# Performance work log

Measured on AMD Instinct MI355X. Metric: run time of the kernel, lower is better.

The kernel has to match this reference:

```python
import math
import jax, jax.numpy as jnp
import numpy as np

B, T, C, H = 4, 2048, 1024, 1024

def setup_inputs() -> dict:
    key = jax.random.key(0)
    kx, kk, kq, kv = jax.random.split(key, 4)
    s = 1.0 / math.sqrt(C)
    return {
        "x": jax.random.normal(kx, (B, T, C), dtype=jnp.float32),
        # torch Linear weight is [out, in]; store transposed [in, out] for x @ W
        "Wk": jax.random.uniform(kk, (C, H), dtype=jnp.float32, minval=-s, maxval=s),
        "Wq": jax.random.uniform(kq, (C, H), dtype=jnp.float32, minval=-s, maxval=s),
        "Wv": jax.random.uniform(kv, (C, H), dtype=jnp.float32, minval=-s, maxval=s),
    }

def reference(x, Wk, Wq, Wv):
    K = x @ Wk  # [B,T,H]
    Q = x @ Wq
    V = x @ Wv
    scale = 1.0 / math.sqrt(K.shape[-1])
    wei = jnp.einsum('bth,bsh->bts', Q, K) * scale  # [B,T,T]
    t = x.shape[1]
    causal = jnp.tril(jnp.ones((t, t), dtype=bool))
    wei = jnp.where(causal, wei, -jnp.inf)
    wei = jax.nn.softmax(wei, axis=-1)
    wei = jax.nn.relu(wei)  # no-op mathematically but kept for fidelity
    return jnp.einsum('bts,bsh->bth', wei, V)
```

## Files before the change

### kernel.cpp

```cpp
#include <hip/hip_runtime.h>

typedef _Float16 f16;
typedef _Float16 f16x8 __attribute__((ext_vector_type(8)));
typedef float    f32x4 __attribute__((ext_vector_type(4)));

#define AS3 __attribute__((address_space(3)))
#define AS1 __attribute__((address_space(1)))

static __device__ __forceinline__ void gld_lds16(const f16* g, f16* l) {
    __builtin_amdgcn_global_load_lds((const AS1 void*)g, (AS3 void*)l, 16, 0, 0);
}

static __device__ __forceinline__ unsigned pack_f16(float a, float b) {
    union { f16 h[2]; unsigned u; } p;
    p.h[0] = (f16)a; p.h[1] = (f16)b;
    return p.u;
}

__global__ void cvt_fused(const float* __restrict__ x, f16* __restrict__ xh,
                          const float* __restrict__ Wq, const float* __restrict__ Wk,
                          const float* __restrict__ Wv, f16* __restrict__ Wt) {
    __shared__ float tile[32][33];
    const int bid = blockIdx.x;
    if (bid < 4096) {
        int i = bid * 256 + threadIdx.x;
        const f32x4* xv = (const f32x4*)x;
        f32x4 a = xv[2 * i], b = xv[2 * i + 1];
        f16x8 h;
        h[0] = (f16)a[0]; h[1] = (f16)a[1]; h[2] = (f16)a[2]; h[3] = (f16)a[3];
        h[4] = (f16)b[0]; h[5] = (f16)b[1]; h[6] = (f16)b[2]; h[7] = (f16)b[3];
        ((f16x8*)xh)[i] = h;
    } else {
        int b2 = bid - 4096;
        int bx = b2 & 31, by = (b2 >> 5) & 31, bz = b2 >> 10;
        const float* W = bz == 0 ? Wq : (bz == 1 ? Wk : Wv);
        int tx = threadIdx.x & 31, ty = threadIdx.x >> 5;
        int n0 = bx * 32, k0 = by * 32;
#pragma unroll
        for (int r = 0; r < 4; ++r)
            tile[ty + r * 8][tx] = W[(size_t)(k0 + ty + r * 8) * 1024 + n0 + tx];
        __syncthreads();
        f16* o = Wt + (size_t)bz * 1024 * 1024;
#pragma unroll
        for (int r = 0; r < 4; ++r)
            o[(size_t)(n0 + ty + r * 8) * 1024 + k0 + tx] = (f16)tile[tx][ty + r * 8];
    }
}

#define KT 16

__global__ __launch_bounds__(512, 2)
void gemm256(const f16* __restrict__ Axh, const f16* __restrict__ Bw, f16* __restrict__ Cqk,
             const f16* __restrict__ Awv, const f16* __restrict__ Bxh, f16* __restrict__ CVt) {
    const int orig = blockIdx.x;
    const int wg = (orig & 7) * 48 + (orig >> 3);
    int m0, n0; const f16 *Ab, *Bb; f16* Cb;
    if (wg < 256) {
        m0 = (wg >> 3) * 256; n0 = (wg & 7) * 256;
        Ab = Axh; Bb = Bw; Cb = Cqk;
    } else {
        int t = wg - 256, bb = t >> 5, r = t & 31;
        m0 = (r >> 3) * 256; n0 = (r & 7) * 256;
        Ab = Awv; Bb = Bxh + (long)bb * 2048 * 1024; Cb = CVt + (long)bb * 1024 * 2048;
    }
    const int lda = 1024, ldb = 1024, ldc = 2048;

    __shared__ f16 lds[2 * 32768];

    const int tid = threadIdx.x;
    const int wave = tid >> 6, lane = tid & 63;
    const int q = lane >> 4, rr = lane & 15;
    const int wr = wave >> 2, wc = wave & 3;

    const int kcs = (((lane & 7) - (lane >> 3)) & 7) * 8;
    const f16* pA = Ab + (long)(m0 + (tid >> 3)) * lda + kcs;
    const f16* pB = Bb + (long)(n0 + (tid >> 3)) * ldb + kcs;
    const int ldsw = wave * 512;

    auto stageA = [&](int kt, int h, int buf) {
        f16* dst = lds + buf * 32768 + h * 8192 + ldsw;
        const f16* src = pA + (long)(h * 128) * lda + kt * 64;
        gld_lds16(src, dst);
        gld_lds16(src + (long)64 * lda, dst + 4096);
    };
    auto stageB = [&](int kt, int h, int buf) {
        f16* dst = lds + buf * 32768 + 16384 + h * 8192 + ldsw;
        const f16* src = pB + (long)(h * 128) * ldb + kt * 64;
        gld_lds16(src, dst);
        gld_lds16(src + (long)64 * ldb, dst + 4096);
    };

    f32x4 acc[8][4] = {};

    stageA(0, 0, 0); stageA(0, 1, 0); stageB(0, 0, 0); stageB(0, 1, 0);
    stageB(1 < KT ? 1 : KT - 1, 0, 1); stageB(1 < KT ? 1 : KT - 1, 1, 1);
    asm volatile("s_waitcnt vmcnt(4)" ::: "memory");
    __builtin_amdgcn_s_barrier();

    for (int u = 0; u < KT; ++u) {
        const int cur = u & 1;
        const f16* bA = lds + cur * 32768 + wr * 8192;
        const f16* bB = lds + cur * 32768 + 16384 + (wc >> 1) * 8192;
        const int brow = (wc & 1) * 64;
        const int ua = u + 1 < KT ? u + 1 : KT - 1;
        const int ub = u + 2 < KT ? u + 2 : KT - 1;
        const int bufA_ = (u + 1) & 1, bufB_ = cur;
        f16x8 bf[4][2];
#pragma unroll
        for (int p = 0; p < 4; ++p) {
            f16x8 a[2][2];
            if (p == 0) {
#pragma unroll
                for (int j = 0; j < 4; ++j)
#pragma unroll
                    for (int ks = 0; ks < 2; ++ks)
                        bf[j][ks] = *(const f16x8*)&bB[(brow + j * 16 + rr) * 64 + ((ks * 4 + q + rr) & 7) * 8];
            }
#pragma unroll
            for (int fi = 0; fi < 2; ++fi)
#pragma unroll
                for (int ks = 0; ks < 2; ++ks)
                    a[fi][ks] = *(const f16x8*)&bA[((p * 2 + fi) * 16 + rr) * 64 + ((ks * 4 + q + rr) & 7) * 8];
            if      (p == 0) stageA(ua, 0, bufA_);
            else if (p == 1) stageA(ua, 1, bufA_);
            else if (p == 2) stageB(ub, 0, bufB_);
            else             stageB(ub, 1, bufB_);
            __builtin_amdgcn_s_barrier();
            asm volatile("s_waitcnt lgkmcnt(0)" ::: "memory");
            __builtin_amdgcn_sched_barrier(0);
            __builtin_amdgcn_s_setprio(1);
#pragma unroll
            for (int ks = 0; ks < 2; ++ks)
#pragma unroll
                for (int fi = 0; fi < 2; ++fi)
#pragma unroll
                    for (int j = 0; j < 4; ++j)
                        acc[p * 2 + fi][j] = __builtin_amdgcn_mfma_f32_16x16x32_f16(
                            a[fi][ks], bf[j][ks], acc[p * 2 + fi][j], 0, 0, 0);
            __builtin_amdgcn_s_setprio(0);
            if (p == 3) asm volatile("s_waitcnt vmcnt(4)" ::: "memory");
            __builtin_amdgcn_s_barrier();
        }
    }
    asm volatile("s_waitcnt vmcnt(0)" ::: "memory");

#pragma unroll
    for (int i = 0; i < 8; ++i)
#pragma unroll
        for (int r2 = 0; r2 < 4; ++r2) {
            const long row = m0 + wr * 128 + i * 16 + q * 4 + r2;
#pragma unroll
            for (int j = 0; j < 4; ++j)
                Cb[row * ldc + n0 + wc * 64 + j * 16 + rr] = (f16)acc[i][j][r2];
        }
}

template <int MODE>
__global__ __launch_bounds__(256, 4)
void gemm128(const f16* __restrict__ A, int lda, long aStride,
             const f16* __restrict__ B, int ldb, long bStride,
             void* __restrict__ Cout, int ldc, long cStride,
             int ktiles, float scale,
             const f16* __restrict__ A2, const f16* __restrict__ B2,
             void* __restrict__ C2) {
    int bm, bn, bz = blockIdx.z;
    int m0, n0;
    const f16 *Ab, *Bb;
    char* Cb;

    if (MODE == 1) {
        int i = blockIdx.x;
        float ff = sqrtf(8.f * (float)i + 1.f);
        bm = (int)((ff - 1.f) * 0.5f);
        while ((bm + 1) * (bm + 2) / 2 <= i) ++bm;
        while (bm * (bm + 1) / 2 > i) --bm;
        bn = i - bm * (bm + 1) / 2;
        m0 = bm * 128; n0 = bn * 128;
        Ab = A + (long)bz * aStride;
        Bb = B + (long)bz * bStride;
        Cb = (char*)Cout + (long)bz * cStride * sizeof(f16);
    } else {
        bn = blockIdx.x; bm = gridDim.y - 1 - blockIdx.y;
        int lim = 4 * (bm + 1); if (lim < ktiles) ktiles = lim;
        m0 = bm * 128; n0 = bn * 128;
        Ab = A + (long)bz * aStride;
        Bb = B + (long)bz * bStride;
        Cb = (char*)Cout + (long)bz * cStride * sizeof(float);
    }

    __shared__ f16 lds[2 * 8192];

    const int tid = threadIdx.x;
    const int wave = tid >> 6, lane = tid & 63;
    const int q = lane >> 4, rr = lane & 15;
    const int wm = (wave >> 1) * 64, wn = (wave & 1) * 64;

    const int kcs = (((tid & 3) - (lane >> 4)) & 3) * 8;
    const f16* pA = Ab + (long)(m0 + (tid >> 2)) * lda + kcs;
    const f16* pB = Bb + (long)(n0 + (tid >> 2)) * ldb + kcs;

    auto stage = [&](int kt, int buf) {
        const int k0 = kt * 32;
        f16* lA = lds + buf * 8192 + wave * 512;
        f16* lB = lds + buf * 8192 + 4096 + wave * 512;
#pragma unroll
        for (int it = 0; it < 2; ++it) {
            gld_lds16(pA + (long)it * 64 * lda + k0, lA + it * 2048);
            gld_lds16(pB + (long)it * 64 * ldb + k0, lB + it * 2048);
        }
    };

    const int slotf = ((q + (rr >> 2)) & 3) * 8;

    f32x4 acc[4][4] = {};
    f32x4 accs[4] = {};
    f16x8 onef;
    const bool sumwave = (MODE == 2) && (wn == 0);
    if (MODE == 2) {
#pragma unroll
        for (int t = 0; t < 8; ++t) onef[t] = (f16)1.0f;
    }

    stage(0, 0);
    __syncthreads();

    for (int kt = 0; kt < ktiles; ++kt) {
        const int cur = kt & 1;
        if (kt + 1 < ktiles) stage(kt + 1, 1 - cur);
        const f16* bufA = lds + cur * 8192;
        const f16* bufB = bufA + 4096;
        f16x8 af[4], bf[4];
#pragma unroll
        for (int i = 0; i < 4; ++i)
            af[i] = *(const f16x8*)&bufA[(wm + i * 16 + rr) * 32 + slotf];
#pragma unroll
        for (int j = 0; j < 4; ++j)
            bf[j] = *(const f16x8*)&bufB[(wn + j * 16 + rr) * 32 + slotf];
#pragma unroll
        for (int i = 0; i < 4; ++i) {
#pragma unroll
            for (int j = 0; j < 4; ++j)
                acc[i][j] = __builtin_amdgcn_mfma_f32_16x16x32_f16(af[i], bf[j], acc[i][j], 0, 0, 0);
            if (sumwave)
                accs[i] = __builtin_amdgcn_mfma_f32_16x16x32_f16(af[i], onef, accs[i], 0, 0, 0);
        }
        __syncthreads();
    }

    float invr[4][4];
    if (MODE == 2) {
        float* rs = (float*)lds;
        if (sumwave && rr == 0) {
#pragma unroll
            for (int i = 0; i < 4; ++i)
#pragma unroll
                for (int r2 = 0; r2 < 4; ++r2)
                    rs[wm + i * 16 + q * 4 + r2] = accs[i][r2];
        }
        __syncthreads();
#pragma unroll
        for (int i = 0; i < 4; ++i)
#pragma unroll
            for (int r2 = 0; r2 < 4; ++r2)
                invr[i][r2] = 1.0f / rs[wm + i * 16 + q * 4 + r2];
    }

#pragma unroll
    for (int i = 0; i < 4; ++i) {
#pragma unroll
        for (int r2 = 0; r2 < 4; ++r2) {
            const int row = wm + i * 16 + q * 4 + r2;
#pragma unroll
            for (int j = 0; j < 4; ++j) {
                const int col = wn + j * 16 + rr;
                float v = acc[i][j][r2] * scale;
                long idx = (long)(m0 + row) * ldc + n0 + col;
                if (MODE == 1) {
                    v = __expf(v);
                    if (n0 + col > m0 + row) v = 0.f;
                    float vo = __shfl_xor(v, 1, 64);
                    if ((rr & 1) == 0)
                        *(unsigned*)((f16*)Cb + idx) = pack_f16(v, vo);
                } else {
                    v *= invr[i][r2];
                    float vo = __shfl_xor(v, 1, 64);
                    if ((rr & 1) == 0)
                        *(float2*)((float*)Cb + idx) = make_float2(v, vo);
                }
            }
        }
    }
}

extern "C" void kernel_launch(void* const* d_in, const int* in_sizes, int n_in,
                              void* d_out, int out_size, void* d_ws, size_t ws_size,
                              hipStream_t stream) {
    (void)in_sizes; (void)n_in; (void)out_size; (void)ws_size;
    const float* x  = (const float*)d_in[0];
    const float* Wk = (const float*)d_in[1];
    const float* Wq = (const float*)d_in[2];
    const float* Wv = (const float*)d_in[3];
    float* out = (float*)d_out;

    const long MB = 1l << 20;
    char* ws = (char*)d_ws;
    f16*   qk   = (f16*)(ws);
    f16*   Vt   = (f16*)(ws + 32 * MB);
    f16*   P    = (f16*)(ws + 48 * MB);
    f16*   xh   = (f16*)(ws + 81 * MB);
    f16*   Wt   = (f16*)(ws + 97 * MB);

    cvt_fused<<<7168, 256, 0, stream>>>(x, xh, Wq, Wk, Wv, Wt);

    gemm256<<<dim3(384), 512, 0, stream>>>(xh, Wt, qk,
                                           Wt + 2l * 1024 * 1024, xh, Vt);
    gemm128<1><<<dim3(136, 1, 4), 256, 0, stream>>>(qk, 2048, 2048l * 2048,
                                                    qk + 1024, 2048, 2048l * 2048,
                                                    P, 2048, 2048l * 2048, 32, 0.03125f,
                                                    nullptr, nullptr, nullptr);
    gemm128<2><<<dim3(8, 16, 4), 256, 0, stream>>>(P, 2048, 2048l * 2048,
                                                   Vt, 2048, 1024l * 2048,
                                                   out, 1024, 2048l * 1024, 64, 1.0f,
                                                   nullptr, nullptr, nullptr);
}
```

Baseline: 249.0 us.

## Move V projection into causal QK^T launch and remap block orders

The V^T = Wv^T·x^T projection tiles move out of the 256-wide projection GEMM and into the causal QK^T launch as extra 128x128 blocks. This balances the triangular QK^T grid with dense work and leaves gemm256 doing only the Q/K projection. Block indices in the QK^T and PV kernels are remapped with interleaving swizzles, meant to improve L2 locality and spread causal work across CUs. Epilogue stores drop the shuffle-and-pack path for plain scalar stores, which may reduce store efficiency.

```diff
diff --git a/kernel.cpp b/kernel.cpp
--- a/kernel.cpp
+++ b/kernel.cpp
@@ -9,12 +9,6 @@
 
 static __device__ __forceinline__ void gld_lds16(const f16* g, f16* l) {
     __builtin_amdgcn_global_load_lds((const AS1 void*)g, (AS3 void*)l, 16, 0, 0);
-}
-
-static __device__ __forceinline__ unsigned pack_f16(float a, float b) {
-    union { f16 h[2]; unsigned u; } p;
-    p.h[0] = (f16)a; p.h[1] = (f16)b;
-    return p.u;
 }
 
 __global__ void cvt_fused(const float* __restrict__ x, f16* __restrict__ xh,
@@ -50,19 +44,11 @@
 #define KT 16
 
 __global__ __launch_bounds__(512, 2)
-void gemm256(const f16* __restrict__ Axh, const f16* __restrict__ Bw, f16* __restrict__ Cqk,
-             const f16* __restrict__ Awv, const f16* __restrict__ Bxh, f16* __restrict__ CVt) {
+void gemm256(const f16* __restrict__ Axh, const f16* __restrict__ Bw, f16* __restrict__ Cqk) {
     const int orig = blockIdx.x;
-    const int wg = (orig & 7) * 48 + (orig >> 3);
-    int m0, n0; const f16 *Ab, *Bb; f16* Cb;
-    if (wg < 256) {
-        m0 = (wg >> 3) * 256; n0 = (wg & 7) * 256;
-        Ab = Axh; Bb = Bw; Cb = Cqk;
-    } else {
-        int t = wg - 256, bb = t >> 5, r = t & 31;
-        m0 = (r >> 3) * 256; n0 = (r & 7) * 256;
-        Ab = Awv; Bb = Bxh + (long)bb * 2048 * 1024; Cb = CVt + (long)bb * 1024 * 2048;
-    }
+    const int wg = (orig & 7) * 32 + (orig >> 3);
+    const int m0 = (wg >> 3) * 256, n0 = (wg & 7) * 256;
+    const f16* Ab = Axh; const f16* Bb = Bw; f16* Cb = Cqk;
     const int lda = 1024, ldb = 1024, ldc = 2048;
 
     __shared__ f16 lds[2 * 32768];
@@ -93,7 +79,7 @@
     f32x4 acc[8][4] = {};
 
     stageA(0, 0, 0); stageA(0, 1, 0); stageB(0, 0, 0); stageB(0, 1, 0);
-    stageB(1 < KT ? 1 : KT - 1, 0, 1); stageB(1 < KT ? 1 : KT - 1, 1, 1);
+    stageB(1, 0, 1); stageB(1, 1, 1);
     asm volatile("s_waitcnt vmcnt(4)" ::: "memory");
     __builtin_amdgcn_s_barrier();
 
@@ -163,24 +149,40 @@
              int ktiles, float scale,
              const f16* __restrict__ A2, const f16* __restrict__ B2,
              void* __restrict__ C2) {
-    int bm, bn, bz = blockIdx.z;
+    int bz = blockIdx.z;
     int m0, n0;
     const f16 *Ab, *Bb;
     char* Cb;
+    bool proj = false;
 
     if (MODE == 1) {
-        int i = blockIdx.x;
-        float ff = sqrtf(8.f * (float)i + 1.f);
-        bm = (int)((ff - 1.f) * 0.5f);
-        while ((bm + 1) * (bm + 2) / 2 <= i) ++bm;
-        while (bm * (bm + 1) / 2 > i) --bm;
-        bn = i - bm * (bm + 1) / 2;
-        m0 = bm * 128; n0 = bn * 128;
-        Ab = A + (long)bz * aStride;
-        Bb = B + (long)bz * bStride;
-        Cb = (char*)Cout + (long)bz * cStride * sizeof(f16);
+        int x = blockIdx.x;
+        int i = (x & 7) * 33 + (x >> 3);
+        if (i < 136) {
+            float ff = sqrtf(8.f * (float)i + 1.f);
+            int bm = (int)((ff - 1.f) * 0.5f);
+            while ((bm + 1) * (bm + 2) / 2 <= i) ++bm;
+            while (bm * (bm + 1) / 2 > i) --bm;
+            int bn = i - bm * (bm + 1) / 2;
+            m0 = bm * 128; n0 = bn * 128;
+            Ab = A + (long)bz * aStride;
+            Bb = B + (long)bz * bStride;
+            Cb = (char*)Cout + (long)bz * cStride * sizeof(f16);
+        } else {
+            proj = true;
+            int vb = i - 136;
+            m0 = (vb >> 4) * 128;
+            n0 = (vb & 15) * 128;
+            Ab = A2;
+            Bb = B2 + (long)bz * 2048 * 1024;
+            Cb = (char*)C2 + (long)bz * 1024 * 2048 * sizeof(f16);
+            lda = 1024; ldb = 1024; ldc = 2048;
+        }
     } else {
-        bn = blockIdx.x; bm = gridDim.y - 1 - blockIdx.y;
+        int l = blockIdx.x + 8 * blockIdx.y;
+        int c = l & 7, idx = l >> 3;
+        int bm = (idx < 8) ? c : 15 - c;
+        int bn = idx & 7;
         int lim = 4 * (bm + 1); if (lim < ktiles) ktiles = lim;
         m0 = bm * 128; n0 = bn * 128;
         Ab = A + (long)bz * aStride;
@@ -265,6 +267,8 @@
                 invr[i][r2] = 1.0f / rs[wm + i * 16 + q * 4 + r2];
     }
 
+    const float scl = (MODE == 1 && proj) ? 1.0f : scale;
+
 #pragma unroll
     for (int i = 0; i < 4; ++i) {
 #pragma unroll
@@ -273,19 +277,16 @@
 #pragma unroll
             for (int j = 0; j < 4; ++j) {
                 const int col = wn + j * 16 + rr;
-                float v = acc[i][j][r2] * scale;
+                float v = acc[i][j][r2] * scl;
                 long idx = (long)(m0 + row) * ldc + n0 + col;
                 if (MODE == 1) {
-                    v = __expf(v);
-                    if (n0 + col > m0 + row) v = 0.f;
-                    float vo = __shfl_xor(v, 1, 64);
-                    if ((rr & 1) == 0)
-                        *(unsigned*)((f16*)Cb + idx) = pack_f16(v, vo);
+                    if (!proj) {
+                        v = __expf(v);
+                        if (n0 + col > m0 + row) v = 0.f;
+                    }
+                    ((f16*)Cb)[idx] = (f16)v;
                 } else {
-                    v *= invr[i][r2];
-                    float vo = __shfl_xor(v, 1, 64);
-                    if ((rr & 1) == 0)
-                        *(float2*)((float*)Cb + idx) = make_float2(v, vo);
+                    ((float*)Cb)[idx] = v * invr[i][r2];
                 }
             }
         }
@@ -312,12 +313,12 @@
 
     cvt_fused<<<7168, 256, 0, stream>>>(x, xh, Wq, Wk, Wv, Wt);
 
-    gemm256<<<dim3(384), 512, 0, stream>>>(xh, Wt, qk,
-                                           Wt + 2l * 1024 * 1024, xh, Vt);
-    gemm128<1><<<dim3(136, 1, 4), 256, 0, stream>>>(qk, 2048, 2048l * 2048,
+    gemm256<<<dim3(256), 512, 0, stream>>>(xh, Wt, qk);
+
+    gemm128<1><<<dim3(264, 1, 4), 256, 0, stream>>>(qk, 2048, 2048l * 2048,
                                                     qk + 1024, 2048, 2048l * 2048,
                                                     P, 2048, 2048l * 2048, 32, 0.03125f,
-                                                    nullptr, nullptr, nullptr);
+                                                    Wt + 2l * 1024 * 1024, xh, Vt);
     gemm128<2><<<dim3(8, 16, 4), 256, 0, stream>>>(P, 2048, 2048l * 2048,
                                                    Vt, 2048, 1024l * 2048,
                                                    out, 1024, 2048l * 1024, 64, 1.0f,
```

New measurement: 246.5 us. Within noise of the previous version (-1.0%).
